# Kernel optimization log

Measured on AMD Instinct MI355X. Metric: run time of the kernel, lower is better.

The kernel has to match this reference:

```python
import jax, jax.numpy as jnp
import numpy as np

H = 16        # num heads
DH = 128      # head dim
C = 64        # delta-rule chunk size
MAG = 0.5     # mag_weight
GATE_NORM = 16.0
EPS = 1e-6


def setup_inputs() -> dict:
    key = jax.random.key(0)
    ks = jax.random.split(key, 5)
    b, n, d = 2, 1024, H * DH
    s = d ** -0.5
    return {
        "x": jax.random.normal(ks[0], (b, n, d), jnp.float32),
        "Wq": jax.random.normal(ks[1], (d, d), jnp.float32) * s,
        "Wk": jax.random.normal(ks[2], (d, d), jnp.float32) * s,
        "Wv": jax.random.normal(ks[3], (d, d), jnp.float32) * s,
        "Wo": jax.random.normal(ks[4], (d, d), jnp.float32) * s,
    }


def _delta_rule_chunkwise(q, k, v, beta, chunk):
    # q,k,v: [b,h,l,d]; beta: [b,h,l,d] per-dim gate. Chunked DeltaNet parallel form.
    b, h, l, dk = q.shape
    dv = v.shape[-1]
    nc = l // chunk
    q = q * (dk ** -0.5)
    v = v * beta
    k_beta = k * beta
    qc, kc, vc, kbc = (a.reshape(b, h, nc, chunk, -1) for a in (q, k, v, k_beta))
    eye = jnp.eye(chunk, dtype=q.dtype)
    strict = jnp.tril(jnp.ones((chunk, chunk), bool), -1)
    # T = (I + strict_lower(k_beta k^T))^{-1} via triangular solve
    L = jnp.where(strict, kbc @ jnp.swapaxes(kc, -1, -2), 0.0)  # [b,h,nc,C,C]
    T = jax.scipy.linalg.solve_triangular(eye + L, jnp.broadcast_to(eye, L.shape), lower=True)
    u = T @ vc    # [b,h,nc,C,dv]
    w = T @ kbc   # [b,h,nc,C,dk]
    incl = jnp.tril(jnp.ones((chunk, chunk), bool))

    def step(S, inp):
        q_i, k_i, u_i, w_i = inp  # [b,h,C,d]
        u_i = u_i - w_i @ S
        attn = jnp.where(incl, q_i @ jnp.swapaxes(k_i, -1, -2), 0.0)
        o_i = q_i @ S + attn @ u_i
        S = S + jnp.swapaxes(k_i, -1, -2) @ u_i
        return S, o_i

    xs = tuple(jnp.moveaxis(a, 2, 0) for a in (qc, kc, u, w))
    S0 = jnp.zeros((b, h, dk, dv), q.dtype)
    S, o = jax.lax.scan(step, S0, xs)
    o = jnp.moveaxis(o, 0, 2).reshape(b, h, l, dv)
    return o, S


def _heads(t, b, n):
    return t.reshape(b, n, H, DH).transpose(0, 2, 1, 3)


def _base_attn(x, Wq, Wk, Wv, Wo):
    # vanilla causal softmax attention using the shared projections
    b, n, d = x.shape
    q, k, v = _heads(x @ Wq, b, n), _heads(x @ Wk, b, n), _heads(x @ Wv, b, n)
    scores = jnp.einsum('bhqd,bhkd->bhqk', q, k) / np.sqrt(DH).astype(np.float32)
    causal = jnp.tril(jnp.ones((n, n), bool))
    a = jax.nn.softmax(jnp.where(causal, scores, -jnp.inf), axis=-1)
    o = jnp.einsum('bhqk,bhkd->bhqd', a, v)
    return o.transpose(0, 2, 1, 3).reshape(b, n, d) @ Wo


def reference(x, Wq, Wk, Wv, Wo):
    b, n, d = x.shape
    k_raw = x @ Wk
    q = _heads(x @ Wq, b, n)
    k = _heads(k_raw, b, n)
    v = _heads(x @ Wv, b, n)
    g = _heads(k_raw, b, n)  # pool_g is identity: output_size == head_dim*num_kv_heads
    q = jnp.clip(jax.nn.softmax(q, axis=-1), EPS, 1.0 - EPS)
    k = jnp.clip(jax.nn.softmax(k, axis=-1), EPS, 1.0 - EPS)
    g = jnp.clip(jax.nn.log_sigmoid(g) / GATE_NORM, -GATE_NORM, GATE_NORM)
    o_lin, _ = _delta_rule_chunkwise(q.astype(jnp.float32), k.astype(jnp.float32),
                                     v.astype(jnp.float32), g.astype(jnp.float32), C)
    o_lin = o_lin.transpose(0, 2, 1, 3).reshape(b, n, d) @ Wo
    o_base = _base_attn(x, Wq, Wk, Wv, Wo)
    return MAG * o_lin + (1.0 - MAG) * o_base
```

## Files before the change

kernel.cpp:

```cpp
#include <hip/hip_runtime.h>
#include <hip/hip_bf16.h>
#include <math.h>

#define D 2048
#define NROWS 2048
#define NQKV 6144
#define H 16
#define DH 128
#define CHK 64
#define NC 16
#define EPSC 1e-6f
#define RSQDH 0.08838834764831845f

typedef unsigned short ushort_t;
typedef __attribute__((ext_vector_type(4))) float f4_t;
typedef __attribute__((ext_vector_type(8))) short s8_t;
typedef __attribute__((ext_vector_type(8))) _Float16 h8_t;
typedef __attribute__((ext_vector_type(4))) _Float16 h4_t;
typedef __attribute__((ext_vector_type(2))) _Float16 h2_t;
typedef __attribute__((ext_vector_type(4))) unsigned short us4_t;
typedef __attribute__((ext_vector_type(2))) unsigned short us2_t;

#define MFMA16(a, b, c) __builtin_amdgcn_mfma_f32_16x16x32_bf16((a), (b), (c), 0, 0, 0)
#define MFMAH(a, b, c)  __builtin_amdgcn_mfma_f32_16x16x32_f16((a), (b), (c), 0, 0, 0)
#define GLOAD16(g, l) __builtin_amdgcn_global_load_lds((const __attribute__((address_space(1))) unsigned int*)(g), (__attribute__((address_space(3))) unsigned int*)(l), 16, 0, 0)

__device__ __forceinline__ ushort_t f2bf(float f) {
  union { float f; unsigned u; } v; v.f = f;
  unsigned r = (v.u + 0x7fffu + ((v.u >> 16) & 1u)) >> 16;
  return (ushort_t)r;
}
__device__ __forceinline__ float bf2f(ushort_t h) {
  union { unsigned u; float f; } v; v.u = ((unsigned)h) << 16;
  return v.f;
}

__global__ __launch_bounds__(256) void split_h(const float* __restrict__ in,
                                               _Float16* __restrict__ hi) {
  int i = (blockIdx.x * 256 + threadIdx.x) * 4;
  float4 v = *(const float4*)(in + i);
  float vv[4] = {v.x, v.y, v.z, v.w};
  h4_t h;
#pragma unroll
  for (int j = 0; j < 4; j++) h[j] = (_Float16)vv[j];
  *(h4_t*)(hi + i) = h;
}

__global__ __launch_bounds__(256) void wsplit4(const float* __restrict__ Wq,
                                               const float* __restrict__ Wk,
                                               const float* __restrict__ Wv,
                                               const float* __restrict__ Wo,
                                               _Float16* __restrict__ Tqkv,
                                               _Float16* __restrict__ To) {
  __shared__ float t[32][33];
  const int tid = threadIdx.x;
  const int k0 = blockIdx.y * 32, n0 = blockIdx.x * 32;
  const int z = blockIdx.z;
  const float* W = (z == 0) ? Wq : (z == 1) ? Wk : (z == 2) ? Wv : Wo;
  _Float16* T = (z < 3) ? (Tqkv + (size_t)z * D * D) : To;
  const int c = tid & 31, rr = tid >> 5;
#pragma unroll
  for (int p = 0; p < 4; p++) {
    int r = p * 8 + rr;
    t[r][c] = W[(size_t)(k0 + r) * D + n0 + c];
  }
  __syncthreads();
#pragma unroll
  for (int p = 0; p < 4; p++) {
    int r = p * 8 + rr;
    T[(size_t)(n0 + r) * D + k0 + c] = (_Float16)t[c][r];
  }
}

__global__ __launch_bounds__(256) void gemm1(const _Float16* __restrict__ Ah,
                                             const _Float16* __restrict__ Bt,
                                             float* __restrict__ C,
                                             int M, int N, int K) {
  __shared__ __align__(16) ushort_t A_s[2][4096];
  __shared__ __align__(16) ushort_t B_s[2][4096];
  const int tid = threadIdx.x, lane = tid & 63, wid = tid >> 6;
  const int nwg = gridDim.x;
  int bid = blockIdx.x;
  int swz = (bid & 7) * (nwg >> 3) + (bid >> 3);
  const int nbn = N >> 7;
  const int bm = swz / nbn, bn = swz % nbn;
  const int row0 = bm << 7, col0 = bn << 7;
  const int lm = lane & 15, lg = lane >> 4;
  const int wrow = (wid >> 1) * 64, wcol = (wid & 1) * 64;
  const int NT = K >> 5;

  f4_t acc[4][4];
#pragma unroll
  for (int m = 0; m < 4; m++)
#pragma unroll
    for (int n = 0; n < 4; n++) acc[m][n] = (f4_t){0.f, 0.f, 0.f, 0.f};

  auto stage = [&](int buf, int ks) {
    int k0 = ks << 5;
#pragma unroll
    for (int p = 0; p < 2; p++) {
      int c = p * 256 + wid * 64 + lane;
      int r = c >> 2, q = (c & 3) * 8;
      char* la = (char*)&A_s[buf][0] + p * 4096 + wid * 1024;
      GLOAD16(Ah + (size_t)(row0 + r) * K + k0 + q, la);
      char* lb = (char*)&B_s[buf][0] + p * 4096 + wid * 1024;
      GLOAD16(Bt + (size_t)(col0 + r) * K + k0 + q, lb);
    }
  };

  stage(0, 0);
  __syncthreads();
  for (int t = 0; t < NT; t++) {
    int cur = t & 1;
    if (t + 1 < NT) stage(cur ^ 1, t + 1);
    h8_t af[4], bfr[4];
#pragma unroll
    for (int m = 0; m < 4; m++)
      af[m] = *(const h8_t*)&A_s[cur][(wrow + m * 16 + lm) * 32 + lg * 8];
#pragma unroll
    for (int n = 0; n < 4; n++)
      bfr[n] = *(const h8_t*)&B_s[cur][(wcol + n * 16 + lm) * 32 + lg * 8];
#pragma unroll
    for (int m = 0; m < 4; m++)
#pragma unroll
      for (int n = 0; n < 4; n++)
        acc[m][n] = MFMAH(af[m], bfr[n], acc[m][n]);
    __syncthreads();
  }
#pragma unroll
  for (int m = 0; m < 4; m++)
#pragma unroll
    for (int n = 0; n < 4; n++)
#pragma unroll
      for (int r = 0; r < 4; r++)
        C[(size_t)(row0 + wrow + m * 16 + lg * 4 + r) * N + col0 + wcol + n * 16 + lm] = acc[m][n][r];
}

__global__ __launch_bounds__(256) void gemm1h(const _Float16* __restrict__ Ah,
                                              const _Float16* __restrict__ Bt,
                                              _Float16* __restrict__ C,
                                              int M, int N, int K) {
  __shared__ __align__(16) ushort_t A_s[2][4096];
  __shared__ __align__(16) ushort_t B_s[2][4096];
  const int tid = threadIdx.x, lane = tid & 63, wid = tid >> 6;
  const int nwg = gridDim.x;
  int bid = blockIdx.x;
  int swz = (bid & 7) * (nwg >> 3) + (bid >> 3);
  const int nbn = N >> 7;
  const int bm = swz / nbn, bn = swz % nbn;
  const int lm = lane & 15, lg = lane >> 4;
  const int row0 = bm << 7, col0 = bn << 7;
  const int wrow = (wid >> 1) * 64, wcol = (wid & 1) * 64;
  const int NT = K >> 5;

  f4_t acc[4][4];
#pragma unroll
  for (int m = 0; m < 4; m++)
#pragma unroll
    for (int n = 0; n < 4; n++) acc[m][n] = (f4_t){0.f, 0.f, 0.f, 0.f};

  auto stage = [&](int buf, int ks) {
    int k0 = ks << 5;
#pragma unroll
    for (int p = 0; p < 2; p++) {
      int c = p * 256 + wid * 64 + lane;
      int r = c >> 2, q = (c & 3) * 8;
      char* la = (char*)&A_s[buf][0] + p * 4096 + wid * 1024;
      GLOAD16(Ah + (size_t)(row0 + r) * K + k0 + q, la);
      char* lb = (char*)&B_s[buf][0] + p * 4096 + wid * 1024;
      GLOAD16(Bt + (size_t)(col0 + r) * K + k0 + q, lb);
    }
  };

  stage(0, 0);
  __syncthreads();
  for (int t = 0; t < NT; t++) {
    int cur = t & 1;
    if (t + 1 < NT) stage(cur ^ 1, t + 1);
    h8_t af[4], bfr[4];
#pragma unroll
    for (int m = 0; m < 4; m++)
      af[m] = *(const h8_t*)&A_s[cur][(wrow + m * 16 + lm) * 32 + lg * 8];
#pragma unroll
    for (int n = 0; n < 4; n++)
      bfr[n] = *(const h8_t*)&B_s[cur][(wcol + n * 16 + lm) * 32 + lg * 8];
#pragma unroll
    for (int m = 0; m < 4; m++)
#pragma unroll
      for (int n = 0; n < 4; n++)
        acc[m][n] = MFMAH(af[m], bfr[n], acc[m][n]);
    __syncthreads();
  }
#pragma unroll
  for (int m = 0; m < 4; m++)
#pragma unroll
    for (int n = 0; n < 4; n++)
#pragma unroll
      for (int r = 0; r < 4; r++)
        C[(size_t)(row0 + wrow + m * 16 + lg * 4 + r) * N + col0 + wcol + n * 16 + lm] = (_Float16)acc[m][n][r];
}

__device__ __forceinline__ float gate_fn(float z) {
  float t = -z;
  float sp = (t > 20.f) ? t : log1pf(expf(t));
  float g = -sp * (1.f / 16.f);
  return fminf(fmaxf(g, -16.f), 16.f);
}

__global__ __launch_bounds__(256) void act_kernel(const _Float16* __restrict__ qkv,
                                                  ushort_t* __restrict__ qs_h,
                                                  ushort_t* __restrict__ qs_l,
                                                  float* __restrict__ ksm,
                                                  float* __restrict__ kb,
                                                  float* __restrict__ vb,
                                                  ushort_t* __restrict__ qb16,
                                                  ushort_t* __restrict__ kb16) {
  int wave = blockIdx.x * 4 + (threadIdx.x >> 6);
  int lane = threadIdx.x & 63;
  int row = wave >> 4, h = wave & 15;
  size_t inb = (size_t)row * NQKV + h * 128;
  size_t base = (size_t)wave * 128;
  const int e0 = 2 * lane;

  h2_t qv = *(const h2_t*)(qkv + inb + e0);
  h2_t kv = *(const h2_t*)(qkv + inb + 2048 + e0);
  h2_t vv = *(const h2_t*)(qkv + inb + 4096 + e0);
  float q0 = (float)qv[0], q1 = (float)qv[1];
  float k0 = (float)kv[0], k1 = (float)kv[1];
  float v0 = (float)vv[0], v1 = (float)vv[1];

  us2_t qo = {f2bf(q0 * RSQDH), f2bf(q1 * RSQDH)};
  us2_t ko = {f2bf(k0), f2bf(k1)};
  *(us2_t*)(qb16 + base + e0) = qo;
  *(us2_t*)(kb16 + base + e0) = ko;

  float m = fmaxf(q0, q1);
  for (int o = 1; o < 64; o <<= 1) m = fmaxf(m, __shfl_xor(m, o));
  float e0f = expf(q0 - m), e1f = expf(q1 - m);
  float s = e0f + e1f;
  for (int o = 1; o < 64; o <<= 1) s += __shfl_xor(s, o);
  float inv = 1.f / s;
  float qs0 = fminf(fmaxf(e0f * inv, EPSC), 1.f - EPSC) * RSQDH;
  float qs1 = fminf(fmaxf(e1f * inv, EPSC), 1.f - EPSC) * RSQDH;

  float mk = fmaxf(k0, k1);
  for (int o = 1; o < 64; o <<= 1) mk = fmaxf(mk, __shfl_xor(mk, o));
  float f0 = expf(k0 - mk), f1 = expf(k1 - mk);
  float sk = f0 + f1;
  for (int o = 1; o < 64; o <<= 1) sk += __shfl_xor(sk, o);
  float invk = 1.f / sk;
  float ks0 = fminf(fmaxf(f0 * invk, EPSC), 1.f - EPSC);
  float ks1 = fminf(fmaxf(f1 * invk, EPSC), 1.f - EPSC);

  float g0 = gate_fn(k0), g1 = gate_fn(k1);

  ushort_t qh0 = f2bf(qs0), qh1 = f2bf(qs1);
  us2_t qhv = {qh0, qh1};
  us2_t qlv = {f2bf(qs0 - bf2f(qh0)), f2bf(qs1 - bf2f(qh1))};
  *(us2_t*)(qs_h + base + e0) = qhv;
  *(us2_t*)(qs_l + base + e0) = qlv;

  *(float2*)(ksm + base + e0) = make_float2(ks0, ks1);
  *(float2*)(kb + base + e0) = make_float2(ks0 * g0, ks1 * g1);
  *(float2*)(vb + base + e0) = make_float2(v0 * g0, v1 * g1);
}

__global__ __launch_bounds__(256) void k_transpose(const float* __restrict__ ksm,
                                                   ushort_t* __restrict__ kTh,
                                                   ushort_t* __restrict__ kTl) {
  __shared__ float t[32][33];
  const int tid = threadIdx.x;
  const int n0 = blockIdx.x * 32;
  const int d0 = blockIdx.y * 32;
  const int bh = blockIdx.z;
  const int b = bh >> 4, h = bh & 15;
  const int c = tid & 31, rr = tid >> 5;
#pragma unroll
  for (int p = 0; p < 4; p++) {
    int r = p * 8 + rr;
    t[r][c] = ksm[(size_t)(b * 1024 + n0 + r) * D + h * 128 + d0 + c];
  }
  __syncthreads();
#pragma unroll
  for (int p = 0; p < 4; p++) {
    int r = p * 8 + rr;
    float v = t[c][r];
    ushort_t hb = f2bf(v);
    kTh[(size_t)(bh * 128 + d0 + r) * 1024 + n0 + c] = hb;
    kTl[(size_t)(bh * 128 + d0 + r) * 1024 + n0 + c] = f2bf(v - bf2f(hb));
  }
}

__global__ __launch_bounds__(256) void chunk_uw_kernel(const ushort_t* __restrict__ qs_h,
                                                       const ushort_t* __restrict__ qs_l,
                                                       const float* __restrict__ ksm,
                                                       const float* __restrict__ kb,
                                                       const float* __restrict__ vb,
                                                       float* __restrict__ u,
                                                       ushort_t* __restrict__ w_h,
                                                       ushort_t* __restrict__ w_l,
                                                       ushort_t* __restrict__ attn_h,
                                                       ushort_t* __restrict__ attn_l) {
  __shared__ __align__(16) ushort_t kh_s[8192];
  __shared__ __align__(16) ushort_t kl_s[8192];
  __shared__ __align__(16) ushort_t xh_s[8192];
  __shared__ __align__(16) ushort_t xl_s[8192];
  __shared__ float L_s[4096];
  const int tid = threadIdx.x, lane = tid & 63, wid = tid >> 6;
  const int lm = lane & 15, lg = lane >> 4;
  const int bh = blockIdx.x >> 4, ci = blockIdx.x & 15;
  const int rowbase = (bh >> 4) * 1024 + ci * 64;
  const int colbase = (bh & 15) * 128;
  const size_t gbase = (size_t)rowbase * D + colbase;
  const int wr = (wid >> 1) * 32, wc = (wid & 1) * 32;

  auto stageM = [&](const float* __restrict__ src, ushort_t* dh, ushort_t* dl) {
#pragma unroll
    for (int it = 0; it < 4; it++) {
      int idx = tid + it * 256;
      int r = idx >> 4, c8 = idx & 15;
      const float* g = src + gbase + (size_t)r * D + c8 * 8;
      float4 v0 = *(const float4*)g;
      float4 v1 = *(const float4*)(g + 4);
      float vv[8] = {v0.x, v0.y, v0.z, v0.w, v1.x, v1.y, v1.z, v1.w};
      s8_t hv, lv;
#pragma unroll
      for (int j = 0; j < 8; j++) {
        ushort_t hb = f2bf(vv[j]);
        hv[j] = (short)hb;
        lv[j] = (short)f2bf(vv[j] - bf2f(hb));
      }
      int byo = r * 256 + ((c8 * 16) ^ ((r & 7) << 4));
      *(s8_t*)((char*)dh + byo) = hv;
      *(s8_t*)((char*)dl + byo) = lv;
    }
  };

  auto stageHL = [&](const ushort_t* __restrict__ srcH,
                     const ushort_t* __restrict__ srcL,
                     ushort_t* dh, ushort_t* dl) {
#pragma unroll
    for (int it = 0; it < 4; it++) {
      int idx = tid + it * 256;
      int r = idx >> 4, c8 = idx & 15;
      size_t g = gbase + (size_t)r * D + c8 * 8;
      s8_t hv = *(const s8_t*)(srcH + g);
      s8_t lv = *(const s8_t*)(srcL + g);
      int byo = r * 256 + ((c8 * 16) ^ ((r & 7) << 4));
      *(s8_t*)((char*)dh + byo) = hv;
      *(s8_t*)((char*)dl + byo) = lv;
    }
  };

  auto mm3 = [&](const ushort_t* Ah, const ushort_t* Al,
                 const ushort_t* Bh, const ushort_t* Bl, f4_t acc[2][2]) {
#pragma unroll
    for (int m = 0; m < 2; m++)
#pragma unroll
      for (int n = 0; n < 2; n++) acc[m][n] = (f4_t){0.f, 0.f, 0.f, 0.f};
#pragma unroll
    for (int term = 0; term < 3; term++) {
      const ushort_t* A = (term == 2) ? Al : Ah;
      const ushort_t* Bsrc = (term == 1) ? Bl : Bh;
#pragma unroll
      for (int ks = 0; ks < 4; ks++) {
        s8_t af[2], bf_[2];
#pragma unroll
        for (int m = 0; m < 2; m++) {
          int row = wr + m * 16 + lm;
          int byo = row * 256 + ((ks * 64 + lg * 16) ^ ((row & 7) << 4));
          af[m] = *(const s8_t*)((const char*)A + byo);
        }
#pragma unroll
        for (int n = 0; n < 2; n++) {
          int row = wc + n * 16 + lm;
          int byo = row * 256 + ((ks * 64 + lg * 16) ^ ((row & 7) << 4));
          bf_[n] = *(const s8_t*)((const char*)Bsrc + byo);
        }
#pragma unroll
        for (int m = 0; m < 2; m++)
#pragma unroll
          for (int n = 0; n < 2; n++)
            acc[m][n] = MFMA16(af[m], bf_[n], acc[m][n]);
      }
    }
  };

  stageM(ksm, kh_s, kl_s);
  stageM(kb, xh_s, xl_s);
  __syncthreads();

  f4_t accL[2][2];
  mm3(xh_s, xl_s, kh_s, kl_s, accL);
#pragma unroll
  for (int m = 0; m < 2; m++)
#pragma unroll
    for (int n = 0; n < 2; n++)
#pragma unroll
      for (int r = 0; r < 4; r++) {
        int i = wr + m * 16 + lg * 4 + r;
        int j = wc + n * 16 + lm;
        L_s[i * 64 + j] = (j < i) ? accL[m][n][r] : 0.f;
      }
  __syncthreads();

  stageHL(qs_h, qs_l, xh_s, xl_s);
  __syncthreads();

  f4_t accA[2][2];
  mm3(xh_s, xl_s, kh_s, kl_s, accA);
  ushort_t* abh = attn_h + (size_t)blockIdx.x * 4096;
  ushort_t* abl = attn_l + (size_t)blockIdx.x * 4096;
#pragma unroll
  for (int m = 0; m < 2; m++)
#pragma unroll
    for (int n = 0; n < 2; n++)
#pragma unroll
      for (int r = 0; r < 4; r++) {
        int i = wr + m * 16 + lg * 4 + r;
        int j = wc + n * 16 + lm;
        float val = (j <= i) ? accA[m][n][r] : 0.f;
        ushort_t hb = f2bf(val);
        abh[i * 64 + j] = hb;
        abl[i * 64 + j] = f2bf(val - bf2f(hb));
      }

  float x[64];
  const int c = tid & 127;
  const float* rhs = (tid < 128) ? (vb + gbase + c) : (kb + gbase + c);
#pragma unroll
  for (int j = 0; j < 64; j++) x[j] = rhs[(size_t)j * D];
#pragma unroll
  for (int i = 0; i < 64; i++) {
    float xi = x[i];
#pragma unroll
    for (int r2 = i + 1; r2 < 64; r2++) x[r2] -= L_s[r2 * 64 + i] * xi;
  }
  if (tid < 128) {
#pragma unroll
    for (int j = 0; j < 64; j++) u[gbase + (size_t)j * D + c] = x[j];
  } else {
#pragma unroll
    for (int j = 0; j < 64; j++) {
      ushort_t hb = f2bf(x[j]);
      w_h[gbase + (size_t)j * D + c] = hb;
      w_l[gbase + (size_t)j * D + c] = f2bf(x[j] - bf2f(hb));
    }
  }
}

__global__ __launch_bounds__(512, 2) void scan_kernel(const ushort_t* __restrict__ qs_h,
                                                      const ushort_t* __restrict__ qs_l,
                                                      const float* __restrict__ u,
                                                      const ushort_t* __restrict__ w_h,
                                                      const ushort_t* __restrict__ w_l,
                                                      const ushort_t* __restrict__ kTh_g,
                                                      const ushort_t* __restrict__ kTl_g,
                                                      const ushort_t* __restrict__ ath_g,
                                                      const ushort_t* __restrict__ atl_g,
                                                      float* __restrict__ o_lin) {
  __shared__ __align__(16) ushort_t kT_h[2][8192];
  __shared__ __align__(16) ushort_t kT_l[2][8192];
  __shared__ __align__(16) ushort_t at_h[2][4096];
  __shared__ __align__(16) ushort_t at_l[2][4096];
  __shared__ __align__(16) ushort_t Sh_s[16 * 128];
  __shared__ __align__(16) ushort_t Sl_s[16 * 128];
  __shared__ __align__(16) ushort_t uh_s[16 * 80];
  __shared__ __align__(16) ushort_t ul_s[16 * 80];
  __shared__ __align__(16) float oT[16 * 68];
  const int tid = threadIdx.x;
  const int bh = blockIdx.x;
  const int b = bh >> 4, h = bh & 15;
  const int g = blockIdx.y;
  const int colbase = h * 128;
  const int vcol = h * 128 + g * 16;
  const int lane = tid & 63, wid = tid >> 6;
  const int lm = lane & 15, lg = lane >> 4;
  const int dsub = lane >> 3;
  const int i8x = (lane & 7) ^ dsub;

  for (int i = tid; i < 16 * 128; i += 512) { Sh_s[i] = 0; Sl_s[i] = 0; }

  f4_t acc3[2];
  acc3[0] = (f4_t){0.f, 0.f, 0.f, 0.f};
  acc3[1] = (f4_t){0.f, 0.f, 0.f, 0.f};

  const ushort_t* kThb = kTh_g + (size_t)bh * 128 * 1024;
  const ushort_t* kTlb = kTl_g + (size_t)bh * 128 * 1024;

  auto issue_stage = [&](int buf, int chunk) {
#pragma unroll
    for (int it = 0; it < 2; it++) {
      int seg = it * 8 + wid;
      int d = seg * 8 + dsub;
      size_t goff = (size_t)d * 1024 + chunk * 64 + i8x * 8;
      GLOAD16(kThb + goff, (char*)&kT_h[buf][0] + seg * 1024);
      GLOAD16(kTlb + goff, (char*)&kT_l[buf][0] + seg * 1024);
    }
    {
      int i = wid * 8 + dsub;
      size_t asrc = (size_t)(bh * 16 + chunk) * 4096 + i * 64 + i8x * 8;
      GLOAD16(ath_g + asrc, (char*)&at_h[buf][0] + wid * 1024);
      GLOAD16(atl_g + asrc, (char*)&at_l[buf][0] + wid * 1024);
    }
  };

  const bool isU = (wid < 4);
  const int m0 = (isU ? wid : (wid - 4)) * 16;
  const ushort_t* AsrcH = isU ? w_h : qs_h;
  const ushort_t* AsrcL = isU ? w_l : qs_l;

  s8_t pAh[4], pAl[4];
  float pu[4];
  auto prefetchA = [&](int chunk) {
    const size_t gb = (size_t)(b * 1024 + chunk * 64) * D;
#pragma unroll
    for (int ks = 0; ks < 4; ks++) {
      size_t off = gb + (size_t)(m0 + lm) * D + colbase + ks * 32 + lg * 8;
      pAh[ks] = *(const s8_t*)(AsrcH + off);
      pAl[ks] = *(const s8_t*)(AsrcL + off);
    }
    if (isU) {
#pragma unroll
      for (int r = 0; r < 4; r++)
        pu[r] = u[gb + (size_t)(m0 + lg * 4 + r) * D + vcol + lm];
    }
  };

  issue_stage(0, 0);
  prefetchA(0);
  __syncthreads();

  for (int chunk = 0; chunk < 16; chunk++) {
    const int cur = chunk & 1;
    const size_t gbase = (size_t)(b * 1024 + chunk * 64) * D;
    if (chunk + 1 < 16) issue_stage(cur ^ 1, chunk + 1);
    {
      f4_t acc = (f4_t){0.f, 0.f, 0.f, 0.f};
#pragma unroll
      for (int ks = 0; ks < 4; ks++) {
        int byo = (lm * 256 + ks * 64 + lg * 16) ^ ((lm & 7) << 4);
        s8_t sh = *(const s8_t*)((const char*)Sh_s + byo);
        s8_t sl = *(const s8_t*)((const char*)Sl_s + byo);
        acc = MFMA16(pAh[ks], sh, acc);
        acc = MFMA16(pAh[ks], sl, acc);
        acc = MFMA16(pAl[ks], sh, acc);
      }
      if (isU) {
        float res[4];
#pragma unroll
        for (int r = 0; r < 4; r++) res[r] = pu[r] - acc[r];
        us4_t rh, rl;
#pragma unroll
        for (int r = 0; r < 4; r++) {
          ushort_t hb = f2bf(res[r]);
          rh[r] = hb;
          rl[r] = f2bf(res[r] - bf2f(hb));
        }
        *(us4_t*)&uh_s[lm * 80 + m0 + lg * 4] = rh;
        *(us4_t*)&ul_s[lm * 80 + m0 + lg * 4] = rl;
      } else {
        float4 res = {acc[0], acc[1], acc[2], acc[3]};
        *(float4*)&oT[lm * 68 + m0 + lg * 4] = res;
      }
    }
    __syncthreads();
    if (chunk + 1 < 16) prefetchA(chunk + 1);
    if (isU) {
      float4 o0 = *(const float4*)&oT[lm * 68 + m0 + lg * 4];
      f4_t acc2 = (f4_t){o0.x, o0.y, o0.z, o0.w};
#pragma unroll
      for (int ks = 0; ks < 2; ks++) {
        int arow = m0 + lm;
        int abyo = arow * 128 + ((ks * 64 + lg * 16) ^ ((arow & 7) << 4));
        s8_t afh = *(const s8_t*)((const char*)&at_h[cur][0] + abyo);
        s8_t afl = *(const s8_t*)((const char*)&at_l[cur][0] + abyo);
        s8_t ufh = *(const s8_t*)&uh_s[lm * 80 + ks * 32 + lg * 8];
        s8_t ufl = *(const s8_t*)&ul_s[lm * 80 + ks * 32 + lg * 8];
        acc2 = MFMA16(afh, ufh, acc2);
        acc2 = MFMA16(afh, ufl, acc2);
        acc2 = MFMA16(afl, ufh, acc2);
      }
#pragma unroll
      for (int r = 0; r < 4; r++)
        o_lin[gbase + (size_t)(m0 + lg * 4 + r) * D + vcol + lm] = acc2[r];
    } else {
      const int w3 = wid - 4;
      s8_t ufh0 = *(const s8_t*)&uh_s[lm * 80 + 0 * 32 + lg * 8];
      s8_t ufl0 = *(const s8_t*)&ul_s[lm * 80 + 0 * 32 + lg * 8];
      s8_t ufh1 = *(const s8_t*)&uh_s[lm * 80 + 1 * 32 + lg * 8];
      s8_t ufl1 = *(const s8_t*)&ul_s[lm * 80 + 1 * 32 + lg * 8];
#pragma unroll
      for (int t = 0; t < 2; t++) {
        const int krow = (w3 * 2 + t) * 16 + lm;
        int b0 = krow * 128 + ((0 * 64 + lg * 16) ^ ((krow & 7) << 4));
        int b1 = krow * 128 + ((1 * 64 + lg * 16) ^ ((krow & 7) << 4));
        s8_t kh0 = *(const s8_t*)((const char*)&kT_h[cur][0] + b0);
        s8_t kl0 = *(const s8_t*)((const char*)&kT_l[cur][0] + b0);
        s8_t kh1 = *(const s8_t*)((const char*)&kT_h[cur][0] + b1);
        s8_t kl1 = *(const s8_t*)((const char*)&kT_l[cur][0] + b1);
        acc3[t] = MFMA16(ufh0, kh0, acc3[t]);
        acc3[t] = MFMA16(ufh0, kl0, acc3[t]);
        acc3[t] = MFMA16(ufl0, kh0, acc3[t]);
        acc3[t] = MFMA16(ufh1, kh1, acc3[t]);
        acc3[t] = MFMA16(ufh1, kl1, acc3[t]);
        acc3[t] = MFMA16(ufl1, kh1, acc3[t]);
      }
#pragma unroll
      for (int t = 0; t < 2; t++)
#pragma unroll
        for (int r = 0; r < 4; r++) {
          int c = lg * 4 + r;
          int k = (w3 * 2 + t) * 16 + lm;
          float sval = acc3[t][r];
          ushort_t hb = f2bf(sval);
          int sbyo = (c * 256 + k * 2) ^ ((c & 7) << 4);
          *(ushort_t*)((char*)Sh_s + sbyo) = hb;
          *(ushort_t*)((char*)Sl_s + sbyo) = f2bf(sval - bf2f(hb));
        }
    }
    __syncthreads();
  }
}

__global__ __launch_bounds__(256) void v_transpose(const _Float16* __restrict__ qkv,
                                                   ushort_t* __restrict__ vt) {
  __shared__ float t[32][33];
  const int tid = threadIdx.x;
  const int n0 = blockIdx.x * 32;
  const int d0 = blockIdx.y * 32;
  const int bh = blockIdx.z;
  const int b = bh >> 4, h = bh & 15;
  const int c = tid & 31, rr = tid >> 5;
#pragma unroll
  for (int p = 0; p < 4; p++) {
    int r = p * 8 + rr;
    t[r][c] = (float)qkv[(size_t)(b * 1024 + n0 + r) * NQKV + 4096 + h * 128 + d0 + c];
  }
  __syncthreads();
#pragma unroll
  for (int p = 0; p < 4; p++) {
    int r = p * 8 + rr;
    vt[(size_t)(bh * 128 + d0 + r) * 1024 + n0 + c] = f2bf(t[c][r]);
  }
}

__global__ __launch_bounds__(256) void attn_mfma(const ushort_t* __restrict__ qb,
                                                 const ushort_t* __restrict__ kb,
                                                 const ushort_t* __restrict__ vt,
                                                 const float* __restrict__ o_lin,
                                                 _Float16* __restrict__ mixh) {
  __shared__ __align__(16) ushort_t K_s[8192];
  __shared__ __align__(16) ushort_t V_s[8192];
  __shared__ __align__(16) ushort_t P_s[4][1152];
  const int tid = threadIdx.x;
  const int lane = tid & 63, wid = tid >> 6;
  const int bh = blockIdx.x;
  const int b = bh >> 4, h = bh & 15;
  const int qt = blockIdx.y;
  const int lm = lane & 15, lg = lane >> 4;

  s8_t qf[4];
  const size_t qrowG = (size_t)(b * 1024 + qt * 64 + wid * 16 + lm);
#pragma unroll
  for (int kb4 = 0; kb4 < 4; kb4++)
    qf[kb4] = *(const s8_t*)(qb + qrowG * D + h * 128 + kb4 * 32 + lg * 8);

  f4_t o[8];
#pragma unroll
  for (int n = 0; n < 8; n++) o[n] = (f4_t){0.f, 0.f, 0.f, 0.f};
  float mrow[4] = {-INFINITY, -INFINITY, -INFINITY, -INFINITY};
  float lrow[4] = {0.f, 0.f, 0.f, 0.f};
  const int myq = qt * 64 + wid * 16 + lg * 4;

  for (int kt = 0; kt <= qt; kt++) {
    __syncthreads();
#pragma unroll
    for (int p = 0; p < 4; p++) {
      int c = tid + p * 256;
      int key = c >> 4, dc = c & 15;
      s8_t v = *(const s8_t*)(kb + (size_t)(b * 1024 + kt * 64 + key) * D + h * 128 + dc * 8);
      int byo = key * 256 + ((dc * 16) ^ ((key & 7) << 4));
      *(s8_t*)((char*)K_s + byo) = v;
    }
#pragma unroll
    for (int p = 0; p < 4; p++) {
      int c = tid + p * 256;
      int d = c >> 3, nc = c & 7;
      s8_t v = *(const s8_t*)(vt + (size_t)(bh * 128 + d) * 1024 + kt * 64 + nc * 8);
      int byo = d * 128 + ((nc * 16) ^ ((d & 7) << 4));
      *(s8_t*)((char*)V_s + byo) = v;
    }
    __syncthreads();

    f4_t s[4];
#pragma unroll
    for (int ks = 0; ks < 4; ks++) {
      f4_t a = (f4_t){0.f, 0.f, 0.f, 0.f};
      int key = ks * 16 + lm;
#pragma unroll
      for (int kb4 = 0; kb4 < 4; kb4++) {
        int byo = key * 256 + ((kb4 * 64 + lg * 16) ^ ((key & 7) << 4));
        s8_t kf = *(const s8_t*)((char*)K_s + byo);
        a = MFMA16(qf[kb4], kf, a);
      }
      s[ks] = a;
    }
    if (kt == qt) {
#pragma unroll
      for (int ks = 0; ks < 4; ks++) {
        int key = kt * 64 + ks * 16 + lm;
#pragma unroll
        for (int r = 0; r < 4; r++)
          if (key > myq + r) s[ks][r] = -INFINITY;
      }
    }
    float mloc[4];
#pragma unroll
    for (int r = 0; r < 4; r++) {
      mloc[r] = fmaxf(fmaxf(s[0][r], s[1][r]), fmaxf(s[2][r], s[3][r]));
      mloc[r] = fmaxf(mloc[r], __shfl_xor(mloc[r], 1));
      mloc[r] = fmaxf(mloc[r], __shfl_xor(mloc[r], 2));
      mloc[r] = fmaxf(mloc[r], __shfl_xor(mloc[r], 4));
      mloc[r] = fmaxf(mloc[r], __shfl_xor(mloc[r], 8));
    }
    float scale[4];
#pragma unroll
    for (int r = 0; r < 4; r++) {
      float mn = fmaxf(mrow[r], mloc[r]);
      scale[r] = __expf(mrow[r] - mn);
      mrow[r] = mn;
    }
    float lad[4] = {0.f, 0.f, 0.f, 0.f};
#pragma unroll
    for (int ks = 0; ks < 4; ks++)
#pragma unroll
      for (int r = 0; r < 4; r++) {
        float p = __expf(s[ks][r] - mrow[r]);
        lad[r] += p;
        P_s[wid][(lg * 4 + r) * 72 + ks * 16 + lm] = f2bf(p);
      }
#pragma unroll
    for (int r = 0; r < 4; r++) {
      lad[r] += __shfl_xor(lad[r], 1);
      lad[r] += __shfl_xor(lad[r], 2);
      lad[r] += __shfl_xor(lad[r], 4);
      lad[r] += __shfl_xor(lad[r], 8);
      lrow[r] = lrow[r] * scale[r] + lad[r];
    }
#pragma unroll
    for (int n = 0; n < 8; n++)
#pragma unroll
      for (int r = 0; r < 4; r++) o[n][r] *= scale[r];

    s8_t pf[2];
#pragma unroll
    for (int ksl = 0; ksl < 2; ksl++)
      pf[ksl] = *(const s8_t*)&P_s[wid][lm * 72 + ksl * 32 + lg * 8];
#pragma unroll
    for (int n = 0; n < 8; n++) {
      int d = n * 16 + lm;
#pragma unroll
      for (int ksl = 0; ksl < 2; ksl++) {
        int byo = d * 128 + ((ksl * 64 + lg * 16) ^ ((d & 7) << 4));
        s8_t vf = *(const s8_t*)((char*)V_s + byo);
        o[n] = MFMA16(pf[ksl], vf, o[n]);
      }
    }
  }

  float invl[4];
#pragma unroll
  for (int r = 0; r < 4; r++) invl[r] = 1.f / lrow[r];
#pragma unroll
  for (int n = 0; n < 8; n++)
#pragma unroll
    for (int r = 0; r < 4; r++) {
      size_t G = (size_t)(b * 1024 + qt * 64 + wid * 16 + lg * 4 + r);
      int dcol = h * 128 + n * 16 + lm;
      float mix = 0.5f * (o[n][r] * invl[r]) + 0.5f * o_lin[G * D + dcol];
      mixh[G * D + dcol] = (_Float16)mix;
    }
}

extern "C" void kernel_launch(void* const* d_in, const int* in_sizes, int n_in,
                              void* d_out, int out_size, void* d_ws, size_t ws_size,
                              hipStream_t stream) {
  const float* x  = (const float*)d_in[0];
  const float* Wq = (const float*)d_in[1];
  const float* Wk = (const float*)d_in[2];
  const float* Wv = (const float*)d_in[3];
  const float* Wo = (const float*)d_in[4];
  float* out = (float*)d_out;
  float* ws = (float*)d_ws;

  const size_t B = (size_t)NROWS * D;
  _Float16* qkv = (_Float16*)(ws + 0 * B);
  float* q_s  = ws + 3 * B;
  float* k_sm = ws + 4 * B;
  float* kbuf = ws + 5 * B;
  float* vbuf = ws + 6 * B;
  float* u    = ws + 7 * B;
  float* w    = ws + 8 * B;
  float* o_lin = kbuf;

  _Float16* x_hi = (_Float16*)u;
  _Float16* Wt   = (_Float16*)(ws + 9 * B);
  ushort_t* attn_h = (ushort_t*)(ws + 9 * B);
  ushort_t* attn_l = attn_h + (size_t)2097152;
  ushort_t* kTh_g  = (ushort_t*)(ws + 9 * B + 2097152);
  ushort_t* kTl_g  = (ushort_t*)(ws + 10 * B);
  _Float16* Wo_t   = (_Float16*)(ws + 10 * B + 2097152);
  ushort_t* qs_h = (ushort_t*)q_s;
  ushort_t* qs_l = qs_h + B;
  ushort_t* w_h  = (ushort_t*)w;
  ushort_t* w_l  = w_h + B;
  ushort_t* qb16 = (ushort_t*)(ws + 2 * B);
  ushort_t* kb16 = qb16 + B;
  ushort_t* vt16 = (ushort_t*)vbuf;
  _Float16* mixh = (_Float16*)qkv;

  split_h<<<4096, 256, 0, stream>>>(x, x_hi);
  wsplit4<<<dim3(64, 64, 4), 256, 0, stream>>>(Wq, Wk, Wv, Wo, Wt, Wo_t);
  gemm1h<<<16 * 48, 256, 0, stream>>>(x_hi, Wt, qkv, NROWS, NQKV, D);

  act_kernel<<<8192, 256, 0, stream>>>(qkv, qs_h, qs_l, k_sm, kbuf, vbuf, qb16, kb16);
  k_transpose<<<dim3(32, 4, 32), 256, 0, stream>>>(k_sm, kTh_g, kTl_g);
  chunk_uw_kernel<<<512, 256, 0, stream>>>(qs_h, qs_l, k_sm, kbuf, vbuf, u, w_h, w_l, attn_h, attn_l);
  scan_kernel<<<dim3(32, 8), 512, 0, stream>>>(qs_h, qs_l, u, w_h, w_l, kTh_g, kTl_g, attn_h, attn_l, o_lin);

  v_transpose<<<dim3(32, 4, 32), 256, 0, stream>>>(qkv, vt16);
  attn_mfma<<<dim3(32, 16), 256, 0, stream>>>(qb16, kb16, vt16, o_lin, mixh);

  gemm1<<<16 * 16, 256, 0, stream>>>(mixh, Wo_t, out, NROWS, D, D);
}
```

Measured before the change: 285.5 us.

## Fuse k transpose into chunk_uw kernel and reverse causal attention tile order

Removes the separate k_transpose launch. chunk_uw_kernel now writes the transposed bf16 hi/lo split of the softmaxed keys straight from its swizzled shared-memory tiles, saving one launch and a re-read of k_sm from global memory. The attention kernel also maps blockIdx.y to query tiles in reverse, so the longest causal tiles are scheduled first for better load balance. The fused transpose stores are 2-byte scattered writes with a stride of 1024 per lane group, which could be less coalesced than the old dedicated transpose.

```diff
diff --git a/kernel.cpp b/kernel.cpp
--- a/kernel.cpp
+++ b/kernel.cpp
@@ -265,32 +265,6 @@
   *(float2*)(vb + base + e0) = make_float2(v0 * g0, v1 * g1);
 }
 
-__global__ __launch_bounds__(256) void k_transpose(const float* __restrict__ ksm,
-                                                   ushort_t* __restrict__ kTh,
-                                                   ushort_t* __restrict__ kTl) {
-  __shared__ float t[32][33];
-  const int tid = threadIdx.x;
-  const int n0 = blockIdx.x * 32;
-  const int d0 = blockIdx.y * 32;
-  const int bh = blockIdx.z;
-  const int b = bh >> 4, h = bh & 15;
-  const int c = tid & 31, rr = tid >> 5;
-#pragma unroll
-  for (int p = 0; p < 4; p++) {
-    int r = p * 8 + rr;
-    t[r][c] = ksm[(size_t)(b * 1024 + n0 + r) * D + h * 128 + d0 + c];
-  }
-  __syncthreads();
-#pragma unroll
-  for (int p = 0; p < 4; p++) {
-    int r = p * 8 + rr;
-    float v = t[c][r];
-    ushort_t hb = f2bf(v);
-    kTh[(size_t)(bh * 128 + d0 + r) * 1024 + n0 + c] = hb;
-    kTl[(size_t)(bh * 128 + d0 + r) * 1024 + n0 + c] = f2bf(v - bf2f(hb));
-  }
-}
-
 __global__ __launch_bounds__(256) void chunk_uw_kernel(const ushort_t* __restrict__ qs_h,
                                                        const ushort_t* __restrict__ qs_l,
                                                        const float* __restrict__ ksm,
@@ -300,7 +274,9 @@
                                                        ushort_t* __restrict__ w_h,
                                                        ushort_t* __restrict__ w_l,
                                                        ushort_t* __restrict__ attn_h,
-                                                       ushort_t* __restrict__ attn_l) {
+                                                       ushort_t* __restrict__ attn_l,
+                                                       ushort_t* __restrict__ kTh_g,
+                                                       ushort_t* __restrict__ kTl_g) {
   __shared__ __align__(16) ushort_t kh_s[8192];
   __shared__ __align__(16) ushort_t kl_s[8192];
   __shared__ __align__(16) ushort_t xh_s[8192];
@@ -392,6 +368,22 @@
 
   f4_t accL[2][2];
   mm3(xh_s, xl_s, kh_s, kl_s, accL);
+
+  {
+    const int dw = wid * 32;
+    const int r = lane;
+#pragma unroll
+    for (int i = 0; i < 32; i++) {
+      int d = dw + i;
+      int byo = r * 256 + ((((d >> 3) ^ (r & 7)) << 4)) + (d & 7) * 2;
+      ushort_t hv = *(const ushort_t*)((const char*)kh_s + byo);
+      ushort_t lv = *(const ushort_t*)((const char*)kl_s + byo);
+      size_t go = (size_t)(bh * 128 + d) * 1024 + ci * 64 + r;
+      kTh_g[go] = hv;
+      kTl_g[go] = lv;
+    }
+  }
+
 #pragma unroll
   for (int m = 0; m < 2; m++)
 #pragma unroll
@@ -657,7 +649,7 @@
   const int lane = tid & 63, wid = tid >> 6;
   const int bh = blockIdx.x;
   const int b = bh >> 4, h = bh & 15;
-  const int qt = blockIdx.y;
+  const int qt = (int)(gridDim.y - 1) - (int)blockIdx.y;
   const int lm = lane & 15, lg = lane >> 4;
 
   s8_t qf[4];
@@ -825,8 +817,8 @@
   gemm1h<<<16 * 48, 256, 0, stream>>>(x_hi, Wt, qkv, NROWS, NQKV, D);
 
   act_kernel<<<8192, 256, 0, stream>>>(qkv, qs_h, qs_l, k_sm, kbuf, vbuf, qb16, kb16);
-  k_transpose<<<dim3(32, 4, 32), 256, 0, stream>>>(k_sm, kTh_g, kTl_g);
-  chunk_uw_kernel<<<512, 256, 0, stream>>>(qs_h, qs_l, k_sm, kbuf, vbuf, u, w_h, w_l, attn_h, attn_l);
+  chunk_uw_kernel<<<512, 256, 0, stream>>>(qs_h, qs_l, k_sm, kbuf, vbuf, u, w_h, w_l,
+                                           attn_h, attn_l, kTh_g, kTl_g);
   scan_kernel<<<dim3(32, 8), 512, 0, stream>>>(qs_h, qs_l, u, w_h, w_l, kTh_g, kTl_g, attn_h, attn_l, o_lin);
 
   v_transpose<<<dim3(32, 4, 32), 256, 0, stream>>>(qkv, vt16);
```

Measured after the change: 277.7 us. 2.7% less time.
